# Kernel optimization log

Hardware: AMD Instinct MI355X
Metric: run time of the kernel (lower is better)

Reference implementation:

```python
import jax, jax.numpy as jnp
import numpy as np

H = 16
D_MODEL = 1024
D_K = D_MODEL // H
B = 4
S = 2048
NEG = -1000000000.0


def setup_inputs() -> dict:
    key = jax.random.key(0)
    ks = jax.random.split(key, 12)
    def lin(k):
        # torch nn.Linear default init: U(-1/sqrt(fan_in), 1/sqrt(fan_in))
        bound = 1.0 / np.sqrt(D_MODEL)
        kw, kb = jax.random.split(k)
        W = jax.random.uniform(kw, (D_MODEL, D_MODEL), jnp.float32, -bound, bound)
        b = jax.random.uniform(kb, (D_MODEL,), jnp.float32, -bound, bound)
        return W, b
    Wq, bq = lin(ks[0]); Wk, bk = lin(ks[1]); Wv, bv = lin(ks[2]); Wo, bo = lin(ks[3])
    return {
        "query": jax.random.normal(ks[4], (B, S, D_MODEL), jnp.float32),
        "key": jax.random.normal(ks[5], (B, S, D_MODEL), jnp.float32),
        "value": jax.random.normal(ks[6], (B, S, D_MODEL), jnp.float32),
        "mask": jax.random.randint(ks[7], (B, S, S), 0, 2, jnp.int32),
        "Wq": Wq, "bq": bq, "Wk": Wk, "bk": bk,
        "Wv": Wv, "bv": bv, "Wo": Wo, "bo": bo,
    }


def reference(query, key, value, mask, Wq, bq, Wk, bk, Wv, bv, Wo, bo):
    # project and split heads: [B,S,D] -> [B,H,S,Dk]
    def proj(x, W, b):
        y = x @ W.T + b
        return y.reshape(B, S, H, D_K).transpose(0, 2, 1, 3)
    q = proj(query, Wq, bq)
    k = proj(key, Wk, bk)
    v = proj(value, Wv, bv)
    m = mask[:, None, :, :]  # [B,1,S,S]
    scores = jnp.einsum("bhqd,bhkd->bhqk", q, k) / jnp.sqrt(jnp.float32(D_K))
    scores = jnp.where(m == 0, NEG, scores)
    p_attn = jax.nn.softmax(scores, axis=-1)
    p_attn = jnp.where(m == 0, 0.0, p_attn)  # faithful to second masked_fill
    x = jnp.einsum("bhqk,bhkd->bhqd", p_attn, v)
    x = x.transpose(0, 2, 1, 3).reshape(B, S, D_MODEL)
    return x @ Wo.T + bo
```

## Files before the change

kernel.cpp:

```cpp
#include <hip/hip_runtime.h>

typedef __attribute__((ext_vector_type(8))) short short8;
typedef __attribute__((ext_vector_type(4))) float f32x4;

#define B_ 4
#define S_ 2048
#define H_ 16
#define DM 1024
#define DK 64

#define QSCALE 0.18033688011112042f

__device__ __forceinline__ unsigned short f2b(float f) {
  unsigned int u = __float_as_uint(f);
  u += 0x7fff + ((u >> 16) & 1);
  return (unsigned short)(u >> 16);
}

__device__ __forceinline__ unsigned int cvtpk_bf16(float lo, float hi) {
  unsigned int r;
  asm("v_cvt_pk_bf16_f32 %0, %1, %2" : "=v"(r) : "v"(lo), "v"(hi));
  return r;
}

__device__ __forceinline__ float amd_exp2(float x) {
#if __has_builtin(__builtin_amdgcn_exp2f)
  return __builtin_amdgcn_exp2f(x);
#else
  return exp2f(x);
#endif
}

__device__ __forceinline__ void gload_lds16(const void* g, void* l) {
  __builtin_amdgcn_global_load_lds(
      (const __attribute__((address_space(1))) unsigned int*)g,
      (__attribute__((address_space(3))) unsigned int*)l, 16, 0, 0);
}

__global__ __launch_bounds__(256) void cvt_kernel(
    const float* __restrict__ a0, const float* __restrict__ a1,
    const float* __restrict__ a2, const float* __restrict__ a3,
    unsigned short* __restrict__ out, int n_per) {
  const float* src = (blockIdx.z == 0) ? a0 : (blockIdx.z == 1) ? a1
                   : (blockIdx.z == 2) ? a2 : a3;
  unsigned short* dst = out + (size_t)blockIdx.z * n_per;
  int i = (blockIdx.x * 256 + threadIdx.x) * 8;
  if (i >= n_per) return;
  float4 x0 = *(const float4*)&src[i];
  float4 x1 = *(const float4*)&src[i + 4];
  alignas(16) unsigned short r[8] = {f2b(x0.x), f2b(x0.y), f2b(x0.z), f2b(x0.w),
                                     f2b(x1.x), f2b(x1.y), f2b(x1.z), f2b(x1.w)};
  *(uint4*)&dst[i] = *(const uint4*)r;
}

__global__ __launch_bounds__(256) void expand_kernel(const int* __restrict__ m,
                                                     uint4* __restrict__ out) {
  unsigned int t = blockIdx.x * 256 + threadIdx.x;
  int lr   = t & 15;
  int quad = (t >> 4) & 3;
  int mt   = (t >> 6) & 1;
  int ks   = (t >> 7) & 1;
  int kt   = (t >> 8) & 31;
  int g    = (t >> 13) & 63;
  int b    = t >> 19;
  int q = g * 32 + mt * 16 + lr;
  int kbase = kt * 64 + ks * 32 + quad * 4;
  const int* row = m + (((size_t)(b * 2048 + q)) << 11) + kbase;
  int4 m0 = *(const int4*)row;
  int4 m1 = *(const int4*)(row + 16);
  uint4 r;
  r.x = (m0.x ? 0xFFFFu : 0u) | (m0.y ? 0xFFFF0000u : 0u);
  r.y = (m0.z ? 0xFFFFu : 0u) | (m0.w ? 0xFFFF0000u : 0u);
  r.z = (m1.x ? 0xFFFFu : 0u) | (m1.y ? 0xFFFF0000u : 0u);
  r.w = (m1.z ? 0xFFFFu : 0u) | (m1.w ? 0xFFFF0000u : 0u);
  out[t] = r;
}

__device__ __forceinline__ void gemm128(
    const unsigned short* __restrict__ A, const unsigned short* __restrict__ W,
    const float* __restrict__ bias, float scale, int mode,
    unsigned short* __restrict__ outb, float* __restrict__ outf) {
  __shared__ unsigned short Sh[128 * 132];
  unsigned short* As = Sh;
  unsigned short* Bs = Sh + 128 * 64;
  const int m0 = blockIdx.x * 128;
  const int n0 = blockIdx.y * 128;
  const int t = threadIdx.x;
  const int lane = t & 63, wave = t >> 6;
  const int lr = lane & 15, quad = lane >> 4;
  const int wm = (wave >> 1) * 64, wn = (wave & 1) * 64;
  const int srow = (lane >> 3);
  const int scol = ((lane & 7) ^ srow) * 8;
  const int cs0 = (quad ^ (lr & 7)) * 8;
  const int cs1 = ((4 + quad) ^ (lr & 7)) * 8;

  const f32x4 zv = {0.f, 0.f, 0.f, 0.f};
  f32x4 acc[4][4];
#pragma unroll
  for (int mt = 0; mt < 4; mt++)
#pragma unroll
    for (int nt = 0; nt < 4; nt++) acc[mt][nt] = zv;

  for (int kb = 0; kb < DM; kb += 64) {
    __syncthreads();
#pragma unroll
    for (int i = 0; i < 4; i++) {
      int c = wave * 4 + i;
      int row = c * 8 + srow;
      gload_lds16(&A[(size_t)(m0 + row) * DM + kb + scol], &As[c * 512]);
      gload_lds16(&W[(size_t)(n0 + row) * DM + kb + scol], &Bs[c * 512]);
    }
    __syncthreads();
#pragma unroll
    for (int ks = 0; ks < 2; ks++) {
      const int cc = ks ? cs1 : cs0;
      short8 af[4], bf[4];
#pragma unroll
      for (int mt = 0; mt < 4; mt++)
        af[mt] = *(const short8*)&As[(wm + mt * 16 + lr) * 64 + cc];
#pragma unroll
      for (int nt = 0; nt < 4; nt++)
        bf[nt] = *(const short8*)&Bs[(wn + nt * 16 + lr) * 64 + cc];
#pragma unroll
      for (int mt = 0; mt < 4; mt++)
#pragma unroll
        for (int nt = 0; nt < 4; nt++)
          acc[mt][nt] = __builtin_amdgcn_mfma_f32_16x16x32_bf16(af[mt], bf[nt], acc[mt][nt], 0, 0, 0);
    }
  }

  if (mode == 1) {
    __syncthreads();
#pragma unroll
    for (int mt = 0; mt < 4; mt++) {
#pragma unroll
      for (int nt = 0; nt < 4; nt++) {
        int n = wn + nt * 16 + lr;
        int m = wm + mt * 16 + quad * 4;
        float bn = bias[n0 + n];
        alignas(8) unsigned short p4[4];
#pragma unroll
        for (int reg = 0; reg < 4; reg++)
          p4[reg] = f2b((acc[mt][nt][reg] + bn) * scale);
        *(uint2*)&Sh[n * 132 + m] = *(const uint2*)p4;
      }
    }
    __syncthreads();
    int n = t >> 1, mh = (t & 1) * 64;
    int gn = n0 + n;
    int h = gn >> 6, dk = gn & 63;
    int b = m0 >> 11, s0 = (m0 & (S_ - 1)) + mh;
    size_t obase = (size_t)((b * H_ + h) * 64 + dk) * S_ + s0;
#pragma unroll
    for (int c = 0; c < 8; c++)
      *(uint4*)&outb[obase + c * 8] = *(const uint4*)&Sh[n * 132 + mh + c * 8];
    return;
  }

#pragma unroll
  for (int mt = 0; mt < 4; mt++) {
#pragma unroll
    for (int nt = 0; nt < 4; nt++) {
#pragma unroll
      for (int reg = 0; reg < 4; reg++) {
        int gm = m0 + wm + mt * 16 + quad * 4 + reg;
        int gn = n0 + wn + nt * 16 + lr;
        float v = (acc[mt][nt][reg] + bias[gn]) * scale;
        if (mode == 0) {
          int b = gm >> 11, s = gm & (S_ - 1);
          int h = gn >> 6, dk = gn & 63;
          outb[(((size_t)(b * H_ + h) * S_ + s) << 6) + dk] = f2b(v);
        } else {
          outf[(size_t)gm * DM + gn] = v;
        }
      }
    }
  }
}

__global__ __launch_bounds__(256) void gemm_qkv_kernel(
    const unsigned short* __restrict__ xb, const unsigned short* __restrict__ wb,
    const float* __restrict__ bq, const float* __restrict__ bk, const float* __restrict__ bv,
    unsigned short* __restrict__ q_out, unsigned short* __restrict__ k_out,
    unsigned short* __restrict__ v_out) {
  int z = blockIdx.z;
  const unsigned short* A = xb + (size_t)z * (B_ * S_ * DM);
  const unsigned short* W = wb + (size_t)z * (DM * DM);
  const float* bias = (z == 0) ? bq : (z == 1) ? bk : bv;
  unsigned short* ob = (z == 0) ? q_out : (z == 1) ? k_out : v_out;
  gemm128(A, W, bias, (z == 0) ? QSCALE : 1.0f, (z == 2) ? 1 : 0, ob, nullptr);
}

__global__ __launch_bounds__(256) void gemm_out_kernel(
    const unsigned short* __restrict__ ab, const unsigned short* __restrict__ wb,
    const float* __restrict__ bo, float* __restrict__ out) {
  gemm128(ab, wb + (size_t)3 * (DM * DM), bo, 1.0f, 2, nullptr, out);
}

__global__ __launch_bounds__(256, 4) void attn_kernel(
    const unsigned short* __restrict__ qb, const unsigned short* __restrict__ kb,
    const unsigned short* __restrict__ vt, const uint4* __restrict__ em,
    unsigned short* __restrict__ ao) {
  __shared__ unsigned short Ks[2][64 * 64];
  __shared__ unsigned short Vs[2][64 * 64];
  const int bh = blockIdx.x;
  const int b = bh >> 4, h = bh & 15;
  const int t = threadIdx.x, lane = t & 63, wave = t >> 6;
  const int lr = lane & 15, quad = lane >> 4;
  const int q0 = blockIdx.y * 128 + wave * 32;
  const unsigned short* qp = qb + (size_t)bh * S_ * DK;
  const unsigned short* kp = kb + (size_t)bh * S_ * DK;
  const unsigned short* vp = vt + (size_t)bh * DK * S_;
  const int g = blockIdx.y * 4 + wave;
  const uint4* emrow = em + ((size_t)(b * 64 + g) * 32) * 256 + lane;

  const int trow = t >> 3;
  const int tsw = ((t & 7) ^ (trow & 7)) * 8;
  const int wbase = wave * 512;
  const int c0 = (quad ^ (lr & 7)) * 8;
  const int c1 = ((4 + quad) ^ (lr & 7)) * 8;
  const int brev = ((quad & 1) << 1) | (quad >> 1);
  const int vc0 = (brev ^ (lr & 7)) * 8;
  const int vc1 = ((4 + brev) ^ (lr & 7)) * 8;

  short8 qf[2][2];
#pragma unroll
  for (int mt = 0; mt < 2; mt++)
#pragma unroll
    for (int ks = 0; ks < 2; ks++)
      qf[mt][ks] = *(const short8*)&qp[(size_t)(q0 + mt * 16 + lr) * DK + ks * 32 + quad * 8];

  const f32x4 zv = {0.f, 0.f, 0.f, 0.f};
  short8 ones;
#pragma unroll
  for (int i = 0; i < 8; i++) ones[i] = (short)0x3F80;
  f32x4 oacc[2][4], lacc[2];
#pragma unroll
  for (int mt = 0; mt < 2; mt++) {
    lacc[mt] = zv;
#pragma unroll
    for (int nt = 0; nt < 4; nt++) oacc[mt][nt] = zv;
  }

#define STAGE(KT, BUF) do {                                                   \
    int kb2 = (KT) * 64;                                                      \
    gload_lds16(kp + (size_t)(kb2 + trow) * DK + tsw,      &Ks[BUF][wbase]);  \
    gload_lds16(kp + (size_t)(kb2 + 32 + trow) * DK + tsw, &Ks[BUF][2048 + wbase]); \
    gload_lds16(vp + (size_t)trow * S_ + kb2 + tsw,        &Vs[BUF][wbase]);  \
    gload_lds16(vp + (size_t)(32 + trow) * S_ + kb2 + tsw, &Vs[BUF][2048 + wbase]); \
  } while (0)

  auto body = [&](int kt, int buf) {
    uint4 mm[2][2];
#pragma unroll
    for (int ks = 0; ks < 2; ks++)
#pragma unroll
      for (int mt = 0; mt < 2; mt++)
        mm[ks][mt] = emrow[(size_t)kt * 256 + (ks * 2 + mt) * 64];

#pragma unroll
    for (int ks = 0; ks < 2; ks++) {
      f32x4 sc[2][2];
#pragma unroll
      for (int ntl = 0; ntl < 2; ntl++) {
        int nt = 2 * ks + ntl;
        short8 kf0 = *(const short8*)&Ks[buf][(nt * 16 + lr) * 64 + c0];
        short8 kf1 = *(const short8*)&Ks[buf][(nt * 16 + lr) * 64 + c1];
#pragma unroll
        for (int mt = 0; mt < 2; mt++) {
          f32x4 z = __builtin_amdgcn_mfma_f32_16x16x32_bf16(kf0, qf[mt][0], zv, 0, 0, 0);
          sc[mt][ntl] = __builtin_amdgcn_mfma_f32_16x16x32_bf16(kf1, qf[mt][1], z, 0, 0, 0);
        }
      }
      short8 pf[2];
#pragma unroll
      for (int mt = 0; mt < 2; mt++) {
        float pa[4], pb[4];
#pragma unroll
        for (int r = 0; r < 4; r++) {
          pa[r] = amd_exp2(sc[mt][0][r]);
          pb[r] = amd_exp2(sc[mt][1][r]);
        }
        unsigned int A0 = cvtpk_bf16(pa[0], pa[1]);
        unsigned int A1 = cvtpk_bf16(pa[2], pa[3]);
        unsigned int B0 = cvtpk_bf16(pb[0], pb[1]);
        unsigned int B1 = cvtpk_bf16(pb[2], pb[3]);
        const uint4 mv = mm[ks][mt];
        A0 &= mv.x; A1 &= mv.y; B0 &= mv.z; B1 &= mv.w;
        asm("v_permlane16_swap_b32 %0, %1" : "+v"(A0), "+v"(B0));
        asm("v_permlane16_swap_b32 %0, %1" : "+v"(A1), "+v"(B1));
        union { unsigned int u[4]; short8 s8; } un;
        un.u[0] = A0; un.u[1] = A1; un.u[2] = B0; un.u[3] = B1;
        pf[mt] = un.s8;
      }
#pragma unroll
      for (int mt = 0; mt < 2; mt++)
        lacc[mt] = __builtin_amdgcn_mfma_f32_16x16x32_bf16(pf[mt], ones, lacc[mt], 0, 0, 0);
      const int vc = ks ? vc1 : vc0;
#pragma unroll
      for (int nt = 0; nt < 4; nt++) {
        short8 vf = *(const short8*)&Vs[buf][(nt * 16 + lr) * 64 + vc];
#pragma unroll
        for (int mt = 0; mt < 2; mt++)
          oacc[mt][nt] = __builtin_amdgcn_mfma_f32_16x16x32_bf16(pf[mt], vf, oacc[mt][nt], 0, 0, 0);
      }
    }
  };

  STAGE(0, 0);
  for (int kt = 0; kt < S_ / 64; kt += 2) {
    __syncthreads();
    STAGE(kt + 1, 1);
    body(kt, 0);
    __syncthreads();
    if (kt + 2 < S_ / 64) STAGE(kt + 2, 0);
    body(kt + 1, 1);
  }
#undef STAGE

#pragma unroll
  for (int mt = 0; mt < 2; mt++) {
#pragma unroll
    for (int r = 0; r < 4; r++) {
      float l = lacc[mt][r];
      float inv = (l > 0.f) ? 1.f / l : 0.f;
      int row = q0 + mt * 16 + quad * 4 + r;
#pragma unroll
      for (int nt = 0; nt < 4; nt++)
        ao[((size_t)(b * S_ + row) * DM) + h * 64 + nt * 16 + lr] =
            f2b(oacc[mt][nt][r] * inv);
    }
  }
}

extern "C" void kernel_launch(void* const* d_in, const int* in_sizes, int n_in,
                              void* d_out, int out_size, void* d_ws, size_t ws_size,
                              hipStream_t stream) {
  const float* query = (const float*)d_in[0];
  const float* key   = (const float*)d_in[1];
  const float* value = (const float*)d_in[2];
  const int*   mask  = (const int*)d_in[3];
  const float* Wq = (const float*)d_in[4];
  const float* bq = (const float*)d_in[5];
  const float* Wk = (const float*)d_in[6];
  const float* bk = (const float*)d_in[7];
  const float* Wv = (const float*)d_in[8];
  const float* bv = (const float*)d_in[9];
  const float* Wo = (const float*)d_in[10];
  const float* bo = (const float*)d_in[11];
  float* out = (float*)d_out;
  char* ws = (char*)d_ws;

  unsigned short* qb = (unsigned short*)(ws);
  unsigned short* kbf = (unsigned short*)(ws + 16777216);
  unsigned short* vt = (unsigned short*)(ws + 33554432);
  unsigned short* wb = (unsigned short*)(ws + 50331648);
  unsigned short* xb = (unsigned short*)(ws + 58720256);
  unsigned short* ao = (unsigned short*)(ws + 58720256);
  uint4* em = (uint4*)(ws + 75497472);

  cvt_kernel<<<dim3(4096, 1, 3), 256, 0, stream>>>(query, key, value, nullptr, xb, B_ * S_ * DM);
  cvt_kernel<<<dim3(512, 1, 4), 256, 0, stream>>>(Wq, Wk, Wv, Wo, wb, DM * DM);
  gemm_qkv_kernel<<<dim3(64, 8, 3), 256, 0, stream>>>(xb, wb, bq, bk, bv, qb, kbf, vt);
  expand_kernel<<<dim3(8192), 256, 0, stream>>>(mask, (uint4*)em);
  attn_kernel<<<dim3(64, 16), 256, 0, stream>>>(qb, kbf, vt, em, ao);
  gemm_out_kernel<<<dim3(64, 8), 256, 0, stream>>>(ao, wb, bo, out);
}
```

Baseline: 381.2 us.

## Double-buffer GEMM LDS tiles and merge conversion kernels into one launch

```diff
diff --git a/kernel.cpp b/kernel.cpp
--- a/kernel.cpp
+++ b/kernel.cpp
@@ -37,20 +37,33 @@
       (__attribute__((address_space(3))) unsigned int*)l, 16, 0, 0);
 }
 
-__global__ __launch_bounds__(256) void cvt_kernel(
-    const float* __restrict__ a0, const float* __restrict__ a1,
-    const float* __restrict__ a2, const float* __restrict__ a3,
-    unsigned short* __restrict__ out, int n_per) {
-  const float* src = (blockIdx.z == 0) ? a0 : (blockIdx.z == 1) ? a1
-                   : (blockIdx.z == 2) ? a2 : a3;
-  unsigned short* dst = out + (size_t)blockIdx.z * n_per;
-  int i = (blockIdx.x * 256 + threadIdx.x) * 8;
-  if (i >= n_per) return;
+__global__ __launch_bounds__(256) void prep_kernel(
+    const float* __restrict__ q, const float* __restrict__ k,
+    const float* __restrict__ v, const float* __restrict__ wq,
+    const float* __restrict__ wk, const float* __restrict__ wv,
+    const float* __restrict__ wo, unsigned short* __restrict__ xb,
+    unsigned short* __restrict__ wbo) {
+  int bid = blockIdx.x;
+  const float* src;
+  unsigned short* dst;
+  int i;
+  if (bid < 12288) {
+    int z = bid >> 12;
+    src = (z == 0) ? q : (z == 1) ? k : v;
+    dst = xb + (size_t)z * (B_ * S_ * DM);
+    i = ((bid & 4095) * 256 + threadIdx.x) * 8;
+  } else {
+    int r = bid - 12288;
+    int z = r >> 9;
+    src = (z == 0) ? wq : (z == 1) ? wk : (z == 2) ? wv : wo;
+    dst = wbo + (size_t)z * (DM * DM);
+    i = ((r & 511) * 256 + threadIdx.x) * 8;
+  }
   float4 x0 = *(const float4*)&src[i];
   float4 x1 = *(const float4*)&src[i + 4];
-  alignas(16) unsigned short r[8] = {f2b(x0.x), f2b(x0.y), f2b(x0.z), f2b(x0.w),
-                                     f2b(x1.x), f2b(x1.y), f2b(x1.z), f2b(x1.w)};
-  *(uint4*)&dst[i] = *(const uint4*)r;
+  alignas(16) unsigned short r8[8] = {f2b(x0.x), f2b(x0.y), f2b(x0.z), f2b(x0.w),
+                                      f2b(x1.x), f2b(x1.y), f2b(x1.z), f2b(x1.w)};
+  *(uint4*)&dst[i] = *(const uint4*)r8;
 }
 
 __global__ __launch_bounds__(256) void expand_kernel(const int* __restrict__ m,
@@ -80,9 +93,7 @@
     const unsigned short* __restrict__ A, const unsigned short* __restrict__ W,
     const float* __restrict__ bias, float scale, int mode,
     unsigned short* __restrict__ outb, float* __restrict__ outf) {
-  __shared__ unsigned short Sh[128 * 132];
-  unsigned short* As = Sh;
-  unsigned short* Bs = Sh + 128 * 64;
+  __shared__ unsigned short Sh[2][16384];
   const int m0 = blockIdx.x * 128;
   const int n0 = blockIdx.y * 128;
   const int t = threadIdx.x;
@@ -101,16 +112,20 @@
 #pragma unroll
     for (int nt = 0; nt < 4; nt++) acc[mt][nt] = zv;
 
-  for (int kb = 0; kb < DM; kb += 64) {
-    __syncthreads();
-#pragma unroll
-    for (int i = 0; i < 4; i++) {
-      int c = wave * 4 + i;
-      int row = c * 8 + srow;
-      gload_lds16(&A[(size_t)(m0 + row) * DM + kb + scol], &As[c * 512]);
-      gload_lds16(&W[(size_t)(n0 + row) * DM + kb + scol], &Bs[c * 512]);
-    }
-    __syncthreads();
+#define GSTAGE(KB, BUF) do {                                                   \
+    int kb2 = (KB) * 64;                                                       \
+    _Pragma("unroll")                                                          \
+    for (int i_ = 0; i_ < 4; i_++) {                                           \
+      int c_ = wave * 4 + i_;                      \
+      int row_ = c_ * 8 + srow;                                                \
+      gload_lds16(&A[(size_t)(m0 + row_) * DM + kb2 + scol], &Sh[BUF][c_ * 512]); \
+      gload_lds16(&W[(size_t)(n0 + row_) * DM + kb2 + scol], &Sh[BUF][8192 + c_ * 512]); \
+    }                                                                          \
+  } while (0)
+
+  auto compute = [&](int buf) {
+    const unsigned short* As = &Sh[buf][0];
+    const unsigned short* Bs = &Sh[buf][8192];
 #pragma unroll
     for (int ks = 0; ks < 2; ks++) {
       const int cc = ks ? cs1 : cs0;
@@ -127,9 +142,21 @@
         for (int nt = 0; nt < 4; nt++)
           acc[mt][nt] = __builtin_amdgcn_mfma_f32_16x16x32_bf16(af[mt], bf[nt], acc[mt][nt], 0, 0, 0);
     }
-  }
+  };
+
+  GSTAGE(0, 0);
+  for (int kb = 0; kb < DM / 64; kb += 2) {
+    __syncthreads();
+    if (kb + 1 < DM / 64) GSTAGE(kb + 1, 1);
+    compute(0);
+    __syncthreads();
+    if (kb + 2 < DM / 64) GSTAGE(kb + 2, 0);
+    compute(1);
+  }
+#undef GSTAGE
 
   if (mode == 1) {
+    unsigned short* Ts = &Sh[0][0];
     __syncthreads();
 #pragma unroll
     for (int mt = 0; mt < 4; mt++) {
@@ -142,7 +169,7 @@
 #pragma unroll
         for (int reg = 0; reg < 4; reg++)
           p4[reg] = f2b((acc[mt][nt][reg] + bn) * scale);
-        *(uint2*)&Sh[n * 132 + m] = *(const uint2*)p4;
+        *(uint2*)&Ts[n * 132 + m] = *(const uint2*)p4;
       }
     }
     __syncthreads();
@@ -153,7 +180,7 @@
     size_t obase = (size_t)((b * H_ + h) * 64 + dk) * S_ + s0;
 #pragma unroll
     for (int c = 0; c < 8; c++)
-      *(uint4*)&outb[obase + c * 8] = *(const uint4*)&Sh[n * 132 + mh + c * 8];
+      *(uint4*)&outb[obase + c * 8] = *(const uint4*)&Ts[n * 132 + mh + c * 8];
     return;
   }
 
@@ -359,8 +386,7 @@
   unsigned short* ao = (unsigned short*)(ws + 58720256);
   uint4* em = (uint4*)(ws + 75497472);
 
-  cvt_kernel<<<dim3(4096, 1, 3), 256, 0, stream>>>(query, key, value, nullptr, xb, B_ * S_ * DM);
-  cvt_kernel<<<dim3(512, 1, 4), 256, 0, stream>>>(Wq, Wk, Wv, Wo, wb, DM * DM);
+  prep_kernel<<<dim3(14336), 256, 0, stream>>>(query, key, value, Wq, Wk, Wv, Wo, xb, wb);
   gemm_qkv_kernel<<<dim3(64, 8, 3), 256, 0, stream>>>(xb, wb, bq, bk, bv, qb, kbf, vt);
   expand_kernel<<<dim3(8192), 256, 0, stream>>>(mask, (uint4*)em);
   attn_kernel<<<dim3(64, 16), 256, 0, stream>>>(qb, kbf, vt, em, ao);
```

New measurement: 384.4 us. About the same (+0.8%).
